# Optimization experiments

Hardware: AMD Instinct MI355X
Metric: run time of the kernel (lower is better)

The kernel has to match this reference:

```python
import jax, jax.numpy as jnp
import numpy as np

EPS = 1e-6  # torch.nn.PairwiseDistance default eps, added to the difference vector


def setup_inputs() -> dict:
    key = jax.random.key(0)
    k1, k2, k3 = jax.random.split(key, 3)
    B, L1, L2, D = 4, 4096, 4096, 3
    contour1 = jax.random.normal(k1, (B, L1, D), dtype=jnp.float32)
    contour2 = jax.random.normal(k2, (B, L2, D), dtype=jnp.float32)
    resolution = jax.random.uniform(k3, (1,), dtype=jnp.float32)
    return {"contour1": contour1, "contour2": contour2, "resolution": resolution}


def reference(contour1, contour2, resolution):
    # torch PairwiseDistance(2): dist = ||x1 - x2 + eps||_2 with x1 from contour1,
    # x2 from contour2. Expand ||c1 - c2 + eps||^2 =
    #   ||c1||^2 + ||c2||^2 - 2 c1.c2 + 2*eps*(sum(c1) - sum(c2)) + D*eps^2
    # to avoid materializing the [B, L2, L1, D] repeated tensors.
    D = contour1.shape[-1]
    s1 = jnp.sum(contour1 * contour1, axis=-1)          # [B, L1]
    s2 = jnp.sum(contour2 * contour2, axis=-1)          # [B, L2]
    sum1 = jnp.sum(contour1, axis=-1)                   # [B, L1]
    sum2 = jnp.sum(contour2, axis=-1)                   # [B, L2]
    cross = jnp.einsum('bmd,bld->bml', contour2, contour1)  # [B, L2, L1]
    dist2 = (s2[:, :, None] + s1[:, None, :] - 2.0 * cross
             + 2.0 * EPS * (sum1[:, None, :] - sum2[:, :, None])
             + D * EPS * EPS)
    dist = jnp.sqrt(jnp.maximum(dist2, 0.0))            # [B, L2, L1]
    min_dist = jnp.min(dist, axis=2)                    # [B, L2]
    return jnp.mean(min_dist * resolution, axis=1)      # [B]
```

## Files before the change

### kernel.cpp

```cpp
#include <hip/hip_runtime.h>
#include <math.h>

#define EPS 1e-6f
#define FLT_BIG 3.402823466e+38f

constexpr int BLK = 256;
constexpr int MPT = 4;
constexpr int NCHUNK = 32;
constexpr int MAXCL = 256;
constexpr int NSLICE = 8;

__global__ void __launch_bounds__(BLK)
k_min(const float* __restrict__ c1, const float* __restrict__ c2,
      float* __restrict__ part, int L1, int L2, int CL) {
    __shared__ float4 tile[MAXCL];

    const int b = blockIdx.z;
    const int chunk = blockIdx.y;
    const int l0 = chunk * CL;
    const int nl = min(CL, L1 - l0);

    const float* src = c1 + ((size_t)b * L1 + l0) * 3;
    for (int i = threadIdx.x; i < nl; i += BLK) {
        float x = src[3 * i], y = src[3 * i + 1], z = src[3 * i + 2];
        tile[i] = make_float4(fmaf(x, x, fmaf(y, y, z * z)),
                              -2.0f * x, -2.0f * y, -2.0f * z);
    }
    __syncthreads();

    const int mbase = blockIdx.x * (BLK * MPT) + threadIdx.x;

    float q0[MPT], q1[MPT], q2[MPT], mn[MPT];
    #pragma unroll
    for (int j = 0; j < MPT; ++j) {
        const int m = mbase + j * BLK;
        if (m < L2) {
            const float* q = c2 + ((size_t)b * L2 + m) * 3;
            q0[j] = q[0] - EPS; q1[j] = q[1] - EPS; q2[j] = q[2] - EPS;
        } else {
            q0[j] = q1[j] = q2[j] = 0.0f;
        }
        mn[j] = FLT_BIG;
    }

    #pragma unroll 4
    for (int l = 0; l < nl; ++l) {
        float4 p = tile[l];
        #pragma unroll
        for (int j = 0; j < MPT; ++j) {
            float t = fmaf(p.y, q0[j], p.x);
            t = fmaf(p.z, q1[j], t);
            t = fmaf(p.w, q2[j], t);
            mn[j] = fminf(mn[j], t);
        }
    }

    float* dst = part + ((size_t)b * NCHUNK + chunk) * L2;
    #pragma unroll
    for (int j = 0; j < MPT; ++j) {
        const int m = mbase + j * BLK;
        if (m < L2) {
            const float qq = fmaf(q0[j], q0[j], fmaf(q1[j], q1[j], q2[j] * q2[j]));
            dst[m] = mn[j] + qq;
        }
    }
}

__global__ void __launch_bounds__(BLK)
k_sqsum(const float* __restrict__ part, float* __restrict__ psum,
        int L2, int SL) {
    const int b = blockIdx.y;
    const int slice = blockIdx.x;
    const int m0 = slice * SL;
    const int mend = min(m0 + SL, L2);

    float sum = 0.0f;
    for (int m = m0 + threadIdx.x; m < mend; m += BLK) {
        float v = FLT_BIG;
        #pragma unroll 8
        for (int c = 0; c < NCHUNK; ++c)
            v = fminf(v, part[((size_t)b * NCHUNK + c) * L2 + m]);
        sum += sqrtf(fmaxf(v, 0.0f));
    }

    __shared__ float red[BLK];
    red[threadIdx.x] = sum;
    __syncthreads();
    for (int s = BLK / 2; s > 0; s >>= 1) {
        if (threadIdx.x < s) red[threadIdx.x] += red[threadIdx.x + s];
        __syncthreads();
    }
    if (threadIdx.x == 0) psum[b * NSLICE + slice] = red[0];
}

__global__ void k_final(const float* __restrict__ psum, const float* __restrict__ res,
                        float* __restrict__ out, int B, int L2) {
    const int b = threadIdx.x;
    if (b < B) {
        float s = 0.0f;
        for (int j = 0; j < NSLICE; ++j) s += psum[b * NSLICE + j];
        out[b] = s * res[0] / (float)L2;
    }
}

extern "C" void kernel_launch(void* const* d_in, const int* in_sizes, int n_in,
                              void* d_out, int out_size, void* d_ws, size_t ws_size,
                              hipStream_t stream) {
    const float* c1  = (const float*)d_in[0];
    const float* c2  = (const float*)d_in[1];
    const float* res = (const float*)d_in[2];
    float* out = (float*)d_out;

    const int B = out_size;
    const int D = 3;
    const int L1 = in_sizes[0] / (B * D);
    const int L2 = in_sizes[1] / (B * D);

    float* part = (float*)d_ws;
    float* psum = part + (size_t)B * NCHUNK * L2;

    const int CL = (L1 + NCHUNK - 1) / NCHUNK;
    dim3 g1((L2 + BLK * MPT - 1) / (BLK * MPT), NCHUNK, B);
    k_min<<<g1, BLK, 0, stream>>>(c1, c2, part, L1, L2, CL);

    const int SL = (L2 + NSLICE - 1) / NSLICE;
    dim3 g2(NSLICE, B);
    k_sqsum<<<g2, BLK, 0, stream>>>(part, psum, L2, SL);

    k_final<<<1, 64, 0, stream>>>(psum, res, out, B, L2);
}
```

Baseline: 19.50 us.

## Fuse min-reduce and final mean into one kernel, pair-unroll the distance loop

The separate slice-sum and final kernels are merged into one 1024-thread block per batch that takes the min over chunks, applies sqrt, reduces with wavefront shuffles and writes the scaled mean directly. This drops one kernel launch and the psum round trip through global memory. The inner distance loop now handles two tile points per iteration and combines them with a nested fminf, which shortens the min dependency chain. The cost is that the reduction runs on only B=4 blocks, so far fewer CUs share that memory traffic than with the earlier 32 blocks.

```diff
diff --git a/kernel.cpp b/kernel.cpp
--- a/kernel.cpp
+++ b/kernel.cpp
@@ -8,7 +8,7 @@
 constexpr int MPT = 4;
 constexpr int NCHUNK = 32;
 constexpr int MAXCL = 256;
-constexpr int NSLICE = 8;
+constexpr int RBLK = 1024;
 
 __global__ void __launch_bounds__(BLK)
 k_min(const float* __restrict__ c1, const float* __restrict__ c2,
@@ -43,14 +43,22 @@
         mn[j] = FLT_BIG;
     }
 
-    #pragma unroll 4
-    for (int l = 0; l < nl; ++l) {
+    int l = 0;
+    #pragma unroll 2
+    for (; l + 2 <= nl; l += 2) {
+        float4 pa = tile[l], pb = tile[l + 1];
+        #pragma unroll
+        for (int j = 0; j < MPT; ++j) {
+            float ta = fmaf(pa.w, q2[j], fmaf(pa.z, q1[j], fmaf(pa.y, q0[j], pa.x)));
+            float tb = fmaf(pb.w, q2[j], fmaf(pb.z, q1[j], fmaf(pb.y, q0[j], pb.x)));
+            mn[j] = fminf(mn[j], fminf(ta, tb));
+        }
+    }
+    for (; l < nl; ++l) {
         float4 p = tile[l];
         #pragma unroll
         for (int j = 0; j < MPT; ++j) {
-            float t = fmaf(p.y, q0[j], p.x);
-            t = fmaf(p.z, q1[j], t);
-            t = fmaf(p.w, q2[j], t);
+            float t = fmaf(p.w, q2[j], fmaf(p.z, q1[j], fmaf(p.y, q0[j], p.x)));
             mn[j] = fminf(mn[j], t);
         }
     }
@@ -66,40 +74,35 @@
     }
 }
 
-__global__ void __launch_bounds__(BLK)
-k_sqsum(const float* __restrict__ part, float* __restrict__ psum,
-        int L2, int SL) {
-    const int b = blockIdx.y;
-    const int slice = blockIdx.x;
-    const int m0 = slice * SL;
-    const int mend = min(m0 + SL, L2);
+__global__ void __launch_bounds__(RBLK)
+k_reduce(const float* __restrict__ part, const float* __restrict__ res,
+         float* __restrict__ out, int L2) {
+    const int b = blockIdx.x;
 
     float sum = 0.0f;
-    for (int m = m0 + threadIdx.x; m < mend; m += BLK) {
+    for (int m = threadIdx.x; m < L2; m += RBLK) {
         float v = FLT_BIG;
-        #pragma unroll 8
+        #pragma unroll
         for (int c = 0; c < NCHUNK; ++c)
             v = fminf(v, part[((size_t)b * NCHUNK + c) * L2 + m]);
         sum += sqrtf(fmaxf(v, 0.0f));
     }
 
-    __shared__ float red[BLK];
-    red[threadIdx.x] = sum;
+    #pragma unroll
+    for (int s = 32; s > 0; s >>= 1)
+        sum += __shfl_down(sum, s, 64);
+
+    __shared__ float wred[RBLK / 64];
+    const int wid = threadIdx.x >> 6;
+    const int lane = threadIdx.x & 63;
+    if (lane == 0) wred[wid] = sum;
     __syncthreads();
-    for (int s = BLK / 2; s > 0; s >>= 1) {
-        if (threadIdx.x < s) red[threadIdx.x] += red[threadIdx.x + s];
-        __syncthreads();
-    }
-    if (threadIdx.x == 0) psum[b * NSLICE + slice] = red[0];
-}
 
-__global__ void k_final(const float* __restrict__ psum, const float* __restrict__ res,
-                        float* __restrict__ out, int B, int L2) {
-    const int b = threadIdx.x;
-    if (b < B) {
-        float s = 0.0f;
-        for (int j = 0; j < NSLICE; ++j) s += psum[b * NSLICE + j];
-        out[b] = s * res[0] / (float)L2;
+    if (threadIdx.x == 0) {
+        float tot = 0.0f;
+        #pragma unroll
+        for (int w = 0; w < RBLK / 64; ++w) tot += wred[w];
+        out[b] = tot * res[0] / (float)L2;
     }
 }
 
@@ -117,15 +120,10 @@
     const int L2 = in_sizes[1] / (B * D);
 
     float* part = (float*)d_ws;
-    float* psum = part + (size_t)B * NCHUNK * L2;
 
     const int CL = (L1 + NCHUNK - 1) / NCHUNK;
     dim3 g1((L2 + BLK * MPT - 1) / (BLK * MPT), NCHUNK, B);
     k_min<<<g1, BLK, 0, stream>>>(c1, c2, part, L1, L2, CL);
 
-    const int SL = (L2 + NSLICE - 1) / NSLICE;
-    dim3 g2(NSLICE, B);
-    k_sqsum<<<g2, BLK, 0, stream>>>(part, psum, L2, SL);
-
-    k_final<<<1, 64, 0, stream>>>(psum, res, out, B, L2);
+    k_reduce<<<B, RBLK, 0, stream>>>(part, res, out, L2);
 }
```

New measurement: 21.43 us. 1.1x slower.
